# Optimization experiments

Measured on AMD Instinct MI355X. Metric: run time of the kernel, lower is better.

The kernel has to match this reference:

```python
import jax, jax.numpy as jnp
import numpy as np

N_OBJ, N_P, N2 = 16, 128, 2048
C, H, W = 256, 384, 384
IMG_W, IMG_H = 384.0, 384.0  # img_metas['img_shape'][:2][::-1]
SIM_THR = 0.0
LOSS_WEIGHT = 1.0
COS_EPS = 1e-8  # torch F.cosine_similarity default


def setup_inputs() -> dict:
    key = jax.random.key(0)
    k1, k2, k3, k4 = jax.random.split(key, 4)
    img_size = jnp.array([IMG_W, IMG_H], jnp.float32)
    point_set_1 = jax.random.uniform(k1, (N_OBJ, N_P, 2), jnp.float32) * img_size
    point_set_2 = jax.random.uniform(k2, (N_OBJ, N2, 2), jnp.float32) * img_size
    key_points = jax.random.uniform(k3, (N_OBJ * N_P, 2), jnp.float32) * img_size
    feats = jax.random.normal(k4, (1, C, H, W), jnp.float32)
    return {"point_set_1": point_set_1, "point_set_2": point_set_2,
            "feats": feats, "key_points": key_points}


def _grid_sample(img, pts01):
    # img: [C,H,W]; pts01: [P,2] (x,y) in [0,1]. Bilinear, align_corners=False,
    # zero padding -- matches mmcv point_sample / torch grid_sample.
    Ci, Hi, Wi = img.shape
    g = 2.0 * pts01 - 1.0
    x = ((g[:, 0] + 1.0) * Wi - 1.0) * 0.5
    y = ((g[:, 1] + 1.0) * Hi - 1.0) * 0.5
    x0 = jnp.floor(x)
    y0 = jnp.floor(y)
    wx1 = x - x0
    wy1 = y - y0

    def tap(xi, yi, wgt):
        valid = (xi >= 0) & (xi < Wi) & (yi >= 0) & (yi < Hi)
        xc = jnp.clip(xi, 0, Wi - 1).astype(jnp.int32)
        yc = jnp.clip(yi, 0, Hi - 1).astype(jnp.int32)
        return img[:, yc, xc] * (wgt * valid)[None, :]  # [C,P]

    return (tap(x0, y0, (1 - wx1) * (1 - wy1))
            + tap(x0 + 1, y0, wx1 * (1 - wy1))
            + tap(x0, y0 + 1, (1 - wx1) * wy1)
            + tap(x0 + 1, y0 + 1, wx1 * wy1))  # [C,P]


def reference(point_set_1, point_set_2, feats, key_points):
    img_size = jnp.array([IMG_W, IMG_H], feats.dtype)
    img = feats[0]  # feats.expand() reuses the same map for every object

    # feats_set_1: [n_obj, n_p, C]; feats_set_2: [n_obj, n2, C]
    f1 = _grid_sample(img, key_points / img_size).T.reshape(N_OBJ, N_P, C)
    f2 = _grid_sample(img, (point_set_2 / img_size).reshape(-1, 2)).T.reshape(N_OBJ, N2, C)

    # cosine similarity over channel dim (norms clamped to eps like torch)
    n1 = jnp.maximum(jnp.linalg.norm(f1, axis=-1), COS_EPS)  # [O,P]
    n2 = jnp.maximum(jnp.linalg.norm(f2, axis=-1), COS_EPS)  # [O,N2]
    sims = jnp.einsum('opc,onc->opn', f1, f2) / (n1[..., None] * n2[:, None, :])
    mask = sims >= SIM_THR  # [O,P,N2]

    # pairwise L2 distances between each key point and candidate set
    diff = point_set_1[:, :, None, :] - point_set_2[:, None, :, :]
    d = jnp.linalg.norm(diff, axis=-1)  # [O,P,N2]

    cnt = mask.sum(-1)  # [O,P]
    has = cnt > 0
    dmin = jnp.min(jnp.where(mask, d, jnp.inf), axis=-1)
    dmean = jnp.sum(jnp.where(mask, d, 0.0), axis=-1) / jnp.maximum(cnt, 1)
    # chamfer of a single point vs masked set: (nearest + mean)/2, 'mean' reduction
    m = (point_set_2.sum(axis=(1, 2)) >= 0).astype(d.dtype)  # [O]
    cost = jnp.where(has, 0.5 * (dmin + dmean), 0.0) * m[:, None]  # [O,P]

    dist = (cost.sum(-1) / N_P).mean()
    return dist * LOSS_WEIGHT
```

## Files before the change

### kernel.cpp

```cpp
#include <hip/hip_runtime.h>
#include <hip/hip_bf16.h>
#include <math.h>

#define W_    384
#define H_    384
#define HW_   (384*384)
#define C_    256
#define NOBJ  16
#define NP    128
#define N2    2048
#define NF1   (NOBJ*NP)
#define NPTS  (NOBJ*NP + NOBJ*N2)
#define NG    16
#define NT    8

typedef __attribute__((ext_vector_type(8))) short short8;
typedef __attribute__((ext_vector_type(4))) float f32x4;

__device__ __forceinline__ unsigned short f2bf(float v) {
    unsigned int u = __float_as_uint(v);
    u += 0x7fffu + ((u >> 16) & 1u);
    return (unsigned short)(u >> 16);
}

__global__ __launch_bounds__(256) void k_transpose(const float* __restrict__ feats,
                                                   unsigned short* __restrict__ ftT) {
    __shared__ float tile[64][65];
    int b     = blockIdx.x;
    int pbase = (b % (HW_ / 64)) * 64;
    int cbase = (b / (HW_ / 64)) * 64;
    int t     = threadIdx.x;

    int p4 = (t & 15) * 4;
    int c0 = t >> 4;
    #pragma unroll
    for (int pass = 0; pass < 4; ++pass) {
        int c = c0 + pass * 16;
        float4 v = *(const float4*)(feats + (size_t)(cbase + c) * HW_ + pbase + p4);
        tile[c][p4 + 0] = v.x; tile[c][p4 + 1] = v.y;
        tile[c][p4 + 2] = v.z; tile[c][p4 + 3] = v.w;
    }
    __syncthreads();

    int c8 = (t & 7) * 8;
    int p0 = t >> 3;
    #pragma unroll
    for (int pass = 0; pass < 2; ++pass) {
        int p = p0 + pass * 32;
        unsigned short u[8];
        #pragma unroll
        for (int j = 0; j < 8; ++j) u[j] = f2bf(tile[c8 + j][p]);
        uint4 pk;
        pk.x = (unsigned)u[0] | ((unsigned)u[1] << 16);
        pk.y = (unsigned)u[2] | ((unsigned)u[3] << 16);
        pk.z = (unsigned)u[4] | ((unsigned)u[5] << 16);
        pk.w = (unsigned)u[6] | ((unsigned)u[7] << 16);
        *(uint4*)(ftT + (size_t)(pbase + p) * C_ + cbase + c8) = pk;
    }
}

__global__ __launch_bounds__(256) void k_sample(const float* __restrict__ kpts,
                                                const float* __restrict__ ps2,
                                                const unsigned short* __restrict__ ftT,
                                                unsigned short* __restrict__ f12) {
    int wave  = blockIdx.x * 4 + (threadIdx.x >> 6);
    int lane  = threadIdx.x & 63;
    int half  = lane >> 5;
    int l32   = lane & 31;
    int point = wave * 2 + half;
    int cb    = l32 * 8;

    const float* src = (point < NF1) ? (kpts + (size_t)point * 2)
                                     : (ps2 + (size_t)(point - NF1) * 2);
    float x  = src[0] - 0.5f;
    float y  = src[1] - 0.5f;
    float x0 = floorf(x), y0 = floorf(y);
    int ix0 = (int)x0, iy0 = (int)y0;
    float fx = x - x0, fy = y - y0;

    float a[8] = {0.f, 0.f, 0.f, 0.f, 0.f, 0.f, 0.f, 0.f};
    #pragma unroll
    for (int dy = 0; dy < 2; ++dy) {
        #pragma unroll
        for (int dx = 0; dx < 2; ++dx) {
            int ix = ix0 + dx, iy = iy0 + dy;
            float w = (dx ? fx : 1.f - fx) * (dy ? fy : 1.f - fy);
            if (ix >= 0 && ix < W_ && iy >= 0 && iy < H_) {
                uint4 tv = *(const uint4*)(ftT + ((size_t)(iy * W_ + ix) * C_ + cb));
                a[0] += w * __uint_as_float(tv.x << 16);
                a[1] += w * __uint_as_float(tv.x & 0xffff0000u);
                a[2] += w * __uint_as_float(tv.y << 16);
                a[3] += w * __uint_as_float(tv.y & 0xffff0000u);
                a[4] += w * __uint_as_float(tv.z << 16);
                a[5] += w * __uint_as_float(tv.z & 0xffff0000u);
                a[6] += w * __uint_as_float(tv.w << 16);
                a[7] += w * __uint_as_float(tv.w & 0xffff0000u);
            }
        }
    }
    uint4 pk;
    pk.x = (unsigned)f2bf(a[0]) | ((unsigned)f2bf(a[1]) << 16);
    pk.y = (unsigned)f2bf(a[2]) | ((unsigned)f2bf(a[3]) << 16);
    pk.z = (unsigned)f2bf(a[4]) | ((unsigned)f2bf(a[5]) << 16);
    pk.w = (unsigned)f2bf(a[6]) | ((unsigned)f2bf(a[7]) << 16);
    *(uint4*)(f12 + (size_t)point * C_ + cb) = pk;
}

__global__ __launch_bounds__(256) void k_sample_direct(const float* __restrict__ kpts,
                                                       const float* __restrict__ ps2,
                                                       const float* __restrict__ feats,
                                                       unsigned short* __restrict__ f12) {
    int point = blockIdx.x * 4 + (threadIdx.x >> 6);
    int lane  = threadIdx.x & 63;
    int cb    = lane * 4;

    const float* src = (point < NF1) ? (kpts + (size_t)point * 2)
                                     : (ps2 + (size_t)(point - NF1) * 2);
    float x  = src[0] - 0.5f, y = src[1] - 0.5f;
    float x0 = floorf(x), y0 = floorf(y);
    int ix0 = (int)x0, iy0 = (int)y0;
    float fx = x - x0, fy = y - y0;

    float acc[4] = {0.f, 0.f, 0.f, 0.f};
    #pragma unroll
    for (int dy = 0; dy < 2; ++dy) {
        #pragma unroll
        for (int dx = 0; dx < 2; ++dx) {
            int ix = ix0 + dx, iy = iy0 + dy;
            float w = (dx ? fx : 1.f - fx) * (dy ? fy : 1.f - fy);
            if (ix >= 0 && ix < W_ && iy >= 0 && iy < H_) {
                int base = iy * W_ + ix;
                #pragma unroll
                for (int u = 0; u < 4; ++u)
                    acc[u] += w * feats[(size_t)(cb + u) * HW_ + base];
            }
        }
    }
    ushort4 o;
    o.x = f2bf(acc[0]); o.y = f2bf(acc[1]); o.z = f2bf(acc[2]); o.w = f2bf(acc[3]);
    *(ushort4*)(f12 + (size_t)point * C_ + cb) = o;
}

__global__ __launch_bounds__(256) void k_simdist(const unsigned short* __restrict__ f12,
                                                 const float* __restrict__ ps1,
                                                 const float* __restrict__ ps2,
                                                 float* __restrict__ pmin,
                                                 float* __restrict__ psum,
                                                 float* __restrict__ pcnt) {
    int wid  = blockIdx.x * 4 + (threadIdx.x >> 6);
    int lane = threadIdx.x & 63;
    int ng = wid & 15;
    int pt = (wid >> 4) & 7;
    int o  = wid >> 7;
    int quad = lane >> 4, col = lane & 15;

    const short* f12s = (const short*)f12;
    const short8* aptr =
        (const short8*)(f12s + ((size_t)(o * NP + pt * 16 + col) * C_ + quad * 8));
    short8 a[8];
    #pragma unroll
    for (int kb = 0; kb < 8; ++kb) a[kb] = aptr[kb * 4];

    const float2* ps1v = (const float2*)ps1;
    const float2* ps2v = (const float2*)ps2;
    float pxr[4], pyr[4];
    #pragma unroll
    for (int r = 0; r < 4; ++r) {
        float2 pc = ps1v[o * NP + pt * 16 + quad * 4 + r];
        pxr[r] = pc.x; pyr[r] = pc.y;
    }

    float mn[4] = {INFINITY, INFINITY, INFINITY, INFINITY};
    float sm[4] = {0.f, 0.f, 0.f, 0.f};
    float ct[4] = {0.f, 0.f, 0.f, 0.f};

    for (int t = 0; t < NT; ++t) {
        int nbase = ng * 128 + t * 16;
        const short8* bptr =
            (const short8*)(f12s + ((size_t)(NF1 + o * N2 + nbase + col) * C_ + quad * 8));
        f32x4 acc = {0.f, 0.f, 0.f, 0.f};
        #pragma unroll
        for (int kb = 0; kb < 8; ++kb)
            acc = __builtin_amdgcn_mfma_f32_16x16x32_bf16(a[kb], bptr[kb * 4], acc, 0, 0, 0);

        float2 nc = ps2v[o * N2 + nbase + col];
        #pragma unroll
        for (int r = 0; r < 4; ++r) {
            if (acc[r] >= 0.f) {
                float dx = pxr[r] - nc.x, dy = pyr[r] - nc.y;
                float d  = sqrtf(dx * dx + dy * dy);
                mn[r] = fminf(mn[r], d); sm[r] += d; ct[r] += 1.f;
            }
        }
    }

    #pragma unroll
    for (int r = 0; r < 4; ++r) {
        #pragma unroll
        for (int off = 1; off < 16; off <<= 1) {
            mn[r] = fminf(mn[r], __shfl_xor(mn[r], off, 16));
            sm[r] += __shfl_xor(sm[r], off, 16);
            ct[r] += __shfl_xor(ct[r], off, 16);
        }
    }
    if (col == 0) {
        #pragma unroll
        for (int r = 0; r < 4; ++r) {
            int p   = pt * 16 + quad * 4 + r;
            int idx = (o * NP + p) * NG + ng;
            pmin[idx] = mn[r]; psum[idx] = sm[r]; pcnt[idx] = ct[r];
        }
    }
}

__global__ __launch_bounds__(1024) void k_final(const float* __restrict__ pmin,
                                                const float* __restrict__ psum,
                                                const float* __restrict__ pcnt,
                                                float* __restrict__ out) {
    int t = threadIdx.x;
    float tot = 0.f;
    for (int pair = t; pair < NOBJ * NP; pair += 1024) {
        int base = pair * NG;
        const float4* pm = (const float4*)(pmin + base);
        const float4* ps = (const float4*)(psum + base);
        const float4* pc = (const float4*)(pcnt + base);
        float mn = INFINITY, sm = 0.f, ct = 0.f;
        #pragma unroll
        for (int g4 = 0; g4 < 4; ++g4) {
            float4 a = pm[g4], b = ps[g4], c = pc[g4];
            mn = fminf(mn, fminf(fminf(a.x, a.y), fminf(a.z, a.w)));
            sm += b.x + b.y + b.z + b.w;
            ct += c.x + c.y + c.z + c.w;
        }
        if (ct > 0.f) tot += 0.5f * (mn + sm / ct);
    }
    #pragma unroll
    for (int off = 32; off; off >>= 1) tot += __shfl_xor(tot, off, 64);
    __shared__ float wsum[16];
    if ((t & 63) == 0) wsum[t >> 6] = tot;
    __syncthreads();
    if (t < 64) {
        float v = (t < 16) ? wsum[t] : 0.f;
        #pragma unroll
        for (int off = 8; off; off >>= 1) v += __shfl_xor(v, off, 16);
        if (t == 0) out[0] = v * (1.0f / (NOBJ * NP));
    }
}

extern "C" void kernel_launch(void* const* d_in, const int* in_sizes, int n_in,
                              void* d_out, int out_size, void* d_ws, size_t ws_size,
                              hipStream_t stream) {
    const float* ps1   = (const float*)d_in[0];
    const float* ps2   = (const float*)d_in[1];
    const float* feats = (const float*)d_in[2];
    const float* kpts  = (const float*)d_in[3];
    float* out = (float*)d_out;

    const size_t sz_ftT  = (size_t)HW_ * C_ * sizeof(unsigned short);
    const size_t sz_f12  = (size_t)NPTS * C_ * sizeof(unsigned short);
    const size_t sz_part = (size_t)NOBJ * NP * NG * sizeof(float);

    char* ws = (char*)d_ws;
    if (ws_size >= sz_ftT + sz_f12 + 3 * sz_part) {
        unsigned short* ftT = (unsigned short*)ws;
        unsigned short* f12 = (unsigned short*)(ws + sz_ftT);
        float* pmin = (float*)(ws + sz_ftT + sz_f12);
        float* psum = (float*)(ws + sz_ftT + sz_f12 + sz_part);
        float* pcnt = (float*)(ws + sz_ftT + sz_f12 + 2 * sz_part);

        k_transpose<<<(HW_ / 64) * (C_ / 64), 256, 0, stream>>>(feats, ftT);
        k_sample<<<NPTS / 8, 256, 0, stream>>>(kpts, ps2, ftT, f12);
        k_simdist<<<NOBJ * 8 * NG / 4, 256, 0, stream>>>(f12, ps1, ps2, pmin, psum, pcnt);
        k_final<<<1, 1024, 0, stream>>>(pmin, psum, pcnt, out);
    } else {
        unsigned short* f12 = (unsigned short*)ws;
        float* pmin = (float*)(ws + sz_f12);
        float* psum = (float*)(ws + sz_f12 + sz_part);
        float* pcnt = (float*)(ws + sz_f12 + 2 * sz_part);

        k_sample_direct<<<NPTS / 4, 256, 0, stream>>>(kpts, ps2, feats, f12);
        k_simdist<<<NOBJ * 8 * NG / 4, 256, 0, stream>>>(f12, ps1, ps2, pmin, psum, pcnt);
        k_final<<<1, 1024, 0, stream>>>(pmin, psum, pcnt, out);
    }
}
```

Baseline: 275.0 us.

## Use direct global-to-LDS loads in transpose and double-buffer B fragments in simdist

The transpose kernel now loads feature tiles straight into LDS with global_load_lds and uses an XOR swizzle in place of padding to avoid bank conflicts. The similarity kernel double-buffers the B-operand fragments in registers, so the loads for the next tile overlap the MFMA and distance work on the current one. This targets memory latency in both kernels, at the cost of more registers and swizzle index arithmetic that must stay consistent between writes and reads.

```diff
diff --git a/kernel.cpp b/kernel.cpp
--- a/kernel.cpp
+++ b/kernel.cpp
@@ -23,33 +23,43 @@
     return (unsigned short)(u >> 16);
 }
 
+__device__ __forceinline__ void gload_lds16(const void* g, void* l) {
+    __builtin_amdgcn_global_load_lds(
+        (const __attribute__((address_space(1))) void*)g,
+        (__attribute__((address_space(3))) void*)l, 16, 0, 0);
+}
+
 __global__ __launch_bounds__(256) void k_transpose(const float* __restrict__ feats,
                                                    unsigned short* __restrict__ ftT) {
-    __shared__ float tile[64][65];
+    __shared__ float tile[64 * 64];
     int b     = blockIdx.x;
     int pbase = (b % (HW_ / 64)) * 64;
     int cbase = (b / (HW_ / 64)) * 64;
     int t     = threadIdx.x;
-
-    int p4 = (t & 15) * 4;
-    int c0 = t >> 4;
+    int l     = t & 63;
+    int w     = t >> 6;
+
     #pragma unroll
     for (int pass = 0; pass < 4; ++pass) {
-        int c = c0 + pass * 16;
-        float4 v = *(const float4*)(feats + (size_t)(cbase + c) * HW_ + pbase + p4);
-        tile[c][p4 + 0] = v.x; tile[c][p4 + 1] = v.y;
-        tile[c][p4 + 2] = v.z; tile[c][p4 + 3] = v.w;
-    }
+        int c    = pass * 16 + w * 4 + (l >> 4);
+        int psrc = ((l & 15) * 4) ^ (((c >> 3) & 3) << 3);
+        const float* src = feats + (size_t)(cbase + c) * HW_ + pbase + psrc;
+        float* dst = &tile[pass * 1024 + w * 256];
+        gload_lds16(src, dst);
+    }
+    asm volatile("s_waitcnt vmcnt(0)" ::: "memory");
     __syncthreads();
 
-    int c8 = (t & 7) * 8;
-    int p0 = t >> 3;
+    int c8  = (t & 7) * 8;
+    int p0  = t >> 3;
+    int swz = (t & 3) << 3;
     #pragma unroll
     for (int pass = 0; pass < 2; ++pass) {
-        int p = p0 + pass * 32;
+        int p   = p0 + pass * 32;
+        int psw = p ^ swz;
         unsigned short u[8];
         #pragma unroll
-        for (int j = 0; j < 8; ++j) u[j] = f2bf(tile[c8 + j][p]);
+        for (int j = 0; j < 8; ++j) u[j] = f2bf(tile[(c8 + j) * 64 + psw]);
         uint4 pk;
         pk.x = (unsigned)u[0] | ((unsigned)u[1] << 16);
         pk.y = (unsigned)u[2] | ((unsigned)u[3] << 16);
@@ -141,6 +151,12 @@
     *(ushort4*)(f12 + (size_t)point * C_ + cb) = o;
 }
 
+__device__ __forceinline__ void bload(const short* bbase, int t, short8* dst) {
+    const short8* bp = (const short8*)(bbase + (size_t)t * 16 * C_);
+    #pragma unroll
+    for (int kb = 0; kb < 8; ++kb) dst[kb] = bp[kb * 4];
+}
+
 __global__ __launch_bounds__(256) void k_simdist(const unsigned short* __restrict__ f12,
                                                  const float* __restrict__ ps1,
                                                  const float* __restrict__ ps2,
@@ -161,6 +177,8 @@
     #pragma unroll
     for (int kb = 0; kb < 8; ++kb) a[kb] = aptr[kb * 4];
 
+    const short* bbase = f12s + ((size_t)(NF1 + o * N2 + ng * 128 + col) * C_ + quad * 8);
+
     const float2* ps1v = (const float2*)ps1;
     const float2* ps2v = (const float2*)ps2;
     float pxr[4], pyr[4];
@@ -174,16 +192,12 @@
     float sm[4] = {0.f, 0.f, 0.f, 0.f};
     float ct[4] = {0.f, 0.f, 0.f, 0.f};
 
-    for (int t = 0; t < NT; ++t) {
-        int nbase = ng * 128 + t * 16;
-        const short8* bptr =
-            (const short8*)(f12s + ((size_t)(NF1 + o * N2 + nbase + col) * C_ + quad * 8));
+    auto ctile = [&](int t, short8 (&b)[8]) {
         f32x4 acc = {0.f, 0.f, 0.f, 0.f};
         #pragma unroll
         for (int kb = 0; kb < 8; ++kb)
-            acc = __builtin_amdgcn_mfma_f32_16x16x32_bf16(a[kb], bptr[kb * 4], acc, 0, 0, 0);
-
-        float2 nc = ps2v[o * N2 + nbase + col];
+            acc = __builtin_amdgcn_mfma_f32_16x16x32_bf16(a[kb], b[kb], acc, 0, 0, 0);
+        float2 nc = ps2v[o * N2 + ng * 128 + t * 16 + col];
         #pragma unroll
         for (int r = 0; r < 4; ++r) {
             if (acc[r] >= 0.f) {
@@ -192,6 +206,15 @@
                 mn[r] = fminf(mn[r], d); sm[r] += d; ct[r] += 1.f;
             }
         }
+    };
+
+    short8 b0[8], b1[8];
+    bload(bbase, 0, b0);
+    for (int t = 0; t < NT; t += 2) {
+        bload(bbase, t + 1, b1);
+        ctile(t, b0);
+        if (t + 2 < NT) bload(bbase, t + 2, b0);
+        ctile(t + 1, b1);
     }
 
     #pragma unroll
```

After: 275.4 us. No clear change (+0.1%).
